# Optimization experiments

Measured on AMD Instinct MI355X. Metric: run time of the kernel, lower is better.

The kernel has to match this reference:

```python
import jax, jax.numpy as jnp
import numpy as np

N_NODES = 100000
N_EDGES = 200000
N_FEAT = 300
HIDDEN = 300
NUM_GRAPHS = 2048
NUM_BOND_TYPE = 6
NUM_BOND_DIR = 3


def setup_inputs() -> dict:
    key = jax.random.key(0)
    ks = jax.random.split(key, 12)
    x = jax.random.normal(ks[0], (N_NODES, N_FEAT), dtype=jnp.float32)
    edge_index = jax.random.randint(ks[1], (2, N_EDGES), 0, N_NODES, dtype=jnp.int64)
    edge_attr = jax.random.randint(ks[2], (N_EDGES, 2), 0, NUM_BOND_DIR, dtype=jnp.int64)
    batch = jnp.sort(jax.random.randint(ks[3], (N_NODES,), 0, NUM_GRAPHS, dtype=jnp.int64))
    s = 1.0 / np.sqrt(N_FEAT)
    emb1 = jax.random.normal(ks[4], (NUM_BOND_TYPE, N_FEAT), dtype=jnp.float32) * s
    emb2 = jax.random.normal(ks[5], (NUM_BOND_DIR, N_FEAT), dtype=jnp.float32) * s
    W1 = jax.random.normal(ks[6], (N_FEAT, 2 * N_FEAT), dtype=jnp.float32) * s
    b1 = jnp.zeros((2 * N_FEAT,), dtype=jnp.float32)
    W2 = jax.random.normal(ks[7], (2 * N_FEAT, HIDDEN), dtype=jnp.float32) * (1.0 / np.sqrt(2 * N_FEAT))
    b2 = jnp.zeros((HIDDEN,), dtype=jnp.float32)
    Wfc = jax.random.normal(ks[8], (HIDDEN, HIDDEN), dtype=jnp.float32) * (1.0 / np.sqrt(HIDDEN))
    bfc = jnp.zeros((HIDDEN,), dtype=jnp.float32)
    return {"x": x, "edge_index": edge_index, "edge_attr": edge_attr, "batch": batch,
            "emb1": emb1, "emb2": emb2, "W1": W1, "b1": b1, "W2": W2, "b2": b2,
            "Wfc": Wfc, "bfc": bfc}


def reference(x, edge_index, edge_attr, batch, emb1, emb2, W1, b1, W2, b2, Wfc, bfc):
    n = x.shape[0]
    # add_self_loops(fill_value=0): append N self edges with zero edge_attr
    loop = jnp.arange(n, dtype=edge_index.dtype)
    src = jnp.concatenate([edge_index[0], loop])  # [E+N]
    dst = jnp.concatenate([edge_index[1], loop])
    ea = jnp.concatenate([edge_attr, jnp.zeros((n, 2), dtype=edge_attr.dtype)], axis=0)
    # edge embeddings (shared by both conv layers)
    edge_emb = emb1[ea[:, 0]] + emb2[ea[:, 1]]  # [E+N, F]

    def mlp(h):
        return jax.nn.relu(h @ W1 + b1) @ W2 + b2

    def gin(h):
        # message: x_j + edge_emb, scatter-add at target nodes, then shared MLP
        msg = h[src] + edge_emb
        aggr = jax.ops.segment_sum(msg, dst, num_segments=n)
        return mlp(aggr)

    h = jax.nn.relu(gin(x))
    h = jax.nn.relu(gin(h))
    # global_add_pool over graphs in batch
    g = jax.ops.segment_sum(h, batch, num_segments=NUM_GRAPHS)  # [G, H]
    return g @ Wfc + bfc
```

## Files before the change

### kernel.cpp

```cpp
#include <hip/hip_runtime.h>
#include <hip/hip_bf16.h>

#define NFEAT 300
#define KP 320
#define NGRAPH 2048
#define N1P 640
#define N2P 384
#define NTD 18
#define SCAN_B 2048

typedef __bf16 bf16x8 __attribute__((ext_vector_type(8)));
typedef float  f32x4  __attribute__((ext_vector_type(4)));
typedef unsigned short u16x8 __attribute__((ext_vector_type(8)));

__device__ __forceinline__ unsigned short f2b(float v) {
    union { float f; unsigned u; } x; x.f = v;
    unsigned r = x.u + 0x7fff + ((x.u >> 16) & 1);
    return (unsigned short)(r >> 16);
}
__device__ __forceinline__ float b2f(unsigned short u) {
    union { unsigned u; float f; } x; x.u = ((unsigned)u) << 16;
    return x.f;
}

#define GLD_LDS16(g, l)                                                        \
    __builtin_amdgcn_global_load_lds(                                          \
        (const __attribute__((address_space(1))) void*)(g),                    \
        (__attribute__((address_space(3))) void*)(l), 16, 0, 0)

__global__ __launch_bounds__(256) void k_embc(
    const float* __restrict__ emb1, const float* __restrict__ emb2,
    float* __restrict__ embc)
{
    int t = blockIdx.x * blockDim.x + threadIdx.x;
    if (t >= NTD * KP) return;
    int td = t / KP, c = t % KP;
    int t1 = td / 3, d = td % 3;
    embc[t] = (c < NFEAT) ? emb1[t1 * NFEAT + c] + emb2[d * NFEAT + c] : 0.f;
}

__global__ __launch_bounds__(256) void k_cvtX(
    const float* __restrict__ x, unsigned short* __restrict__ xb, int n, int Mpad)
{
    int idx = blockIdx.x * blockDim.x + threadIdx.x;
    if (idx >= Mpad * (KP / 8)) return;
    int row = idx / (KP / 8), c0 = (idx % (KP / 8)) * 8;
    unsigned short o[8];
#pragma unroll
    for (int j = 0; j < 8; ++j) {
        int col = c0 + j;
        float v = (row < n && col < NFEAT) ? x[(size_t)row * NFEAT + col] : 0.f;
        o[j] = f2b(v);
    }
    *(uint4*)&xb[(size_t)row * KP + c0] = *(uint4*)o;
}

__global__ __launch_bounds__(256) void k_zero(int* __restrict__ p, int n)
{
    int i = blockIdx.x * blockDim.x + threadIdx.x;
    if (i < n) p[i] = 0;
}

__global__ __launch_bounds__(256) void k_deg(
    const int* __restrict__ ei, int* __restrict__ deg, int E)
{
    int e = blockIdx.x * blockDim.x + threadIdx.x;
    if (e >= E) return;
    atomicAdd(&deg[ei[E + e]], 1);
}

__global__ __launch_bounds__(256) void k_scan1(
    const int* __restrict__ deg, int* __restrict__ offsets,
    int* __restrict__ bsum, int n)
{
    __shared__ int sh[256];
    int tid = threadIdx.x;
    int base = blockIdx.x * SCAN_B + tid * 8;
    int v[8], run = 0;
#pragma unroll
    for (int j = 0; j < 8; ++j) {
        int i = base + j;
        v[j] = (i < n) ? deg[i] : 0;
        run += v[j];
        v[j] = run;
    }
    sh[tid] = run;
    __syncthreads();
    for (int off = 1; off < 256; off <<= 1) {
        int t = (tid >= off) ? sh[tid - off] : 0;
        __syncthreads();
        sh[tid] += t;
        __syncthreads();
    }
    int excl = sh[tid] - run;
#pragma unroll
    for (int j = 0; j < 8; ++j) {
        int i = base + j;
        if (i < n) offsets[i + 1] = excl + v[j];
    }
    if (tid == 0) bsum[blockIdx.x] = sh[255];
}

__global__ void k_scan2(int* __restrict__ bsum, int nb, int* __restrict__ offsets)
{
    if (threadIdx.x == 0 && blockIdx.x == 0) {
        int run = 0;
        for (int b = 0; b < nb; ++b) { int t = bsum[b]; bsum[b] = run; run += t; }
        offsets[0] = 0;
    }
}

__global__ __launch_bounds__(256) void k_scan3(
    const int* __restrict__ deg, int* __restrict__ offsets,
    const int* __restrict__ bsum, int* __restrict__ cursor, int n)
{
    int i = blockIdx.x * blockDim.x + threadIdx.x;
    if (i >= n) return;
    int fin = offsets[i + 1] + bsum[i / SCAN_B];
    offsets[i + 1] = fin;
    cursor[i] = fin - deg[i];
}

__global__ __launch_bounds__(256) void k_fill(
    const int* __restrict__ ei, const int* __restrict__ ea,
    int* __restrict__ cursor, int* __restrict__ edgerec, int E)
{
    int e = blockIdx.x * blockDim.x + threadIdx.x;
    if (e >= E) return;
    int dst = ei[E + e];
    int pos = atomicAdd(&cursor[dst], 1);
    int src = ei[e];
    int td  = ea[2 * e] * 3 + ea[2 * e + 1];
    edgerec[pos] = src | (td << 20);
}

__global__ __launch_bounds__(256) void k_aggr(
    const unsigned short* __restrict__ h,
    const int* __restrict__ offsets, const int* __restrict__ edgerec,
    const float* __restrict__ embc,
    unsigned short* __restrict__ Ab, int n, int Mpad)
{
    int idx = blockIdx.x * blockDim.x + threadIdx.x;
    if (idx >= Mpad * (KP / 8)) return;
    int v = idx / (KP / 8), c0 = (idx % (KP / 8)) * 8;
    unsigned short* outp = &Ab[(size_t)v * KP + c0];
    if (v >= n) {
        *(uint4*)outp = make_uint4(0, 0, 0, 0);
        return;
    }
    float acc[8];
    u16x8 hv = *(const u16x8*)&h[(size_t)v * KP + c0];
    const float* e0 = embc + c0;
#pragma unroll
    for (int j = 0; j < 8; ++j) acc[j] = b2f(hv[j]) + e0[j];

    int beg = offsets[v], end = offsets[v + 1];
    for (int e = beg; e < end; ++e) {
        int rec = edgerec[e];
        int src = rec & 0xFFFFF;
        int td  = rec >> 20;
        u16x8 hs = *(const u16x8*)&h[(size_t)src * KP + c0];
        const float* ee = embc + td * KP + c0;
#pragma unroll
        for (int j = 0; j < 8; ++j) acc[j] += b2f(hs[j]) + ee[j];
    }
    unsigned short o[8];
#pragma unroll
    for (int j = 0; j < 8; ++j) o[j] = f2b(acc[j]);
    *(uint4*)outp = *(uint4*)o;
}

__global__ __launch_bounds__(256) void k_cvtW(
    const float* __restrict__ W, unsigned short* __restrict__ Wt,
    int rows, int cols, int Kpad, int Npad)
{
    int t = blockIdx.x * blockDim.x + threadIdx.x;
    if (t >= Npad * Kpad) return;
    int nn = t / Kpad, k = t % Kpad;
    float v = (k < rows && nn < cols) ? W[(size_t)k * cols + nn] : 0.f;
    Wt[t] = f2b(v);
}

__global__ __launch_bounds__(256) void k_gemm(
    const unsigned short* __restrict__ Ag, const unsigned short* __restrict__ Bg,
    const float* __restrict__ bias, int bias_n,
    unsigned short* __restrict__ C, int ldc, int store_cols,
    int K, int npass, int MT)
{
    __shared__ unsigned short smem[8192];

    int tid  = threadIdx.x;
    int lane = tid & 63, wave = tid >> 6;

    int l    = blockIdx.x;
    int xcd  = l & 7;
    int j    = l >> 3;
    int ncol = j % npass;
    int panel= (j / npass) * 8 + xcd;
    if (panel >= MT) return;
    int m0 = panel * 128;

    int wm = (wave >> 1) * 64, wn = (wave & 1) * 64;
    int fr = lane & 15, fq = lane >> 4;
    int colq = lane & 15, rq = (lane >> 4) * 4;

    const unsigned short* Abase = Ag + (size_t)m0 * K;
    const unsigned short* Bbase = Bg + (size_t)ncol * 128 * K;

    int c0 = tid, c1 = 256 + tid;
    size_t aoff0 = (size_t)(c0 >> 2) * K + 8 * ((c0 & 3) ^ ((c0 >> 3) & 3));
    size_t aoff1 = (size_t)(c1 >> 2) * K + 8 * ((c1 & 3) ^ ((c1 >> 3) & 3));

    int fswz = 8 * (fq ^ ((fr >> 1) & 3));

    f32x4 acc[4][4];
#pragma unroll
    for (int i = 0; i < 4; ++i)
#pragma unroll
        for (int jj = 0; jj < 4; ++jj)
            acc[i][jj] = (f32x4){0.f, 0.f, 0.f, 0.f};

    for (int k0 = 0; k0 < K; k0 += 32) {
        GLD_LDS16(Abase + aoff0 + k0, &smem[c0 * 8]);
        GLD_LDS16(Abase + aoff1 + k0, &smem[c1 * 8]);
        GLD_LDS16(Bbase + aoff0 + k0, &smem[4096 + c0 * 8]);
        GLD_LDS16(Bbase + aoff1 + k0, &smem[4096 + c1 * 8]);
        __syncthreads();

        bf16x8 af[4], bfv[4];
#pragma unroll
        for (int i = 0; i < 4; ++i) {
            af[i]  = *(const bf16x8*)&smem[(wm + i * 16 + fr) * 32 + fswz];
            bfv[i] = *(const bf16x8*)&smem[4096 + (wn + i * 16 + fr) * 32 + fswz];
        }
#pragma unroll
        for (int i = 0; i < 4; ++i)
#pragma unroll
            for (int jj = 0; jj < 4; ++jj)
                acc[i][jj] = __builtin_amdgcn_mfma_f32_16x16x32_bf16(
                    af[i], bfv[jj], acc[i][jj], 0, 0, 0);
        __syncthreads();
    }

#pragma unroll
    for (int ch = 0; ch < 2; ++ch) {
        if ((wn >> 6) == ch) {
#pragma unroll
            for (int jj = 0; jj < 4; ++jj) {
                int lc  = jj * 16 + colq;
                int col = ncol * 128 + wn + jj * 16 + colq;
                float bv = (col < bias_n) ? bias[col] : 0.f;
#pragma unroll
                for (int i = 0; i < 4; ++i) {
                    int rbase = wm + i * 16 + rq;
#pragma unroll
                    for (int r = 0; r < 4; ++r) {
                        float v = fmaxf(acc[i][jj][r] + bv, 0.f);
                        smem[(rbase + r) * 64 + lc] = f2b(v);
                    }
                }
            }
        }
        __syncthreads();
        int cbase = ncol * 128 + ch * 64;
        if (cbase < store_cols) {
#pragma unroll
            for (int i = 0; i < 4; ++i) {
                int idx = i * 256 + tid;
                int row = idx >> 3, c8 = idx & 7;
                *(uint4*)&C[(size_t)(m0 + row) * ldc + cbase + c8 * 8] =
                    *(uint4*)&smem[row * 64 + c8 * 8];
            }
        }
        __syncthreads();
    }
}

__global__ __launch_bounds__(256) void k_pool(
    const unsigned short* __restrict__ H, const int* __restrict__ batch,
    float* __restrict__ g, int n)
{
    int gid = blockIdx.x;
    int lo = 0, hi = n;
    while (lo < hi) { int mid = (lo + hi) >> 1; if (batch[mid] < gid) lo = mid + 1; else hi = mid; }
    int start = lo;
    hi = n;
    while (lo < hi) { int mid = (lo + hi) >> 1; if (batch[mid] < gid + 1) lo = mid + 1; else hi = mid; }
    int end = lo;

    for (int f = threadIdx.x; f < NFEAT; f += blockDim.x) {
        float acc = 0.f;
        for (int v = start; v < end; ++v) acc += b2f(H[(size_t)v * KP + f]);
        g[(size_t)gid * NFEAT + f] = acc;
    }
}

__global__ __launch_bounds__(256) void k_final(
    const float* __restrict__ g, const float* __restrict__ Wfc,
    const float* __restrict__ bfc, float* __restrict__ out)
{
    int idx = blockIdx.x * blockDim.x + threadIdx.x;
    if (idx >= NGRAPH * NFEAT) return;
    int r = idx / NFEAT, c = idx % NFEAT;
    float acc = bfc[c];
    for (int k = 0; k < NFEAT; ++k)
        acc = fmaf(g[(size_t)r * NFEAT + k], Wfc[(size_t)k * NFEAT + c], acc);
    out[idx] = acc;
}

extern "C" void kernel_launch(void* const* d_in, const int* in_sizes, int n_in,
                              void* d_out, int out_size, void* d_ws, size_t ws_size,
                              hipStream_t stream)
{
    const float* x    = (const float*)d_in[0];
    const int*   ei   = (const int*)  d_in[1];
    const int*   ea   = (const int*)  d_in[2];
    const int*   batch= (const int*)  d_in[3];
    const float* emb1 = (const float*)d_in[4];
    const float* emb2 = (const float*)d_in[5];
    const float* W1   = (const float*)d_in[6];
    const float* b1   = (const float*)d_in[7];
    const float* W2   = (const float*)d_in[8];
    const float* b2   = (const float*)d_in[9];
    const float* Wfc  = (const float*)d_in[10];
    const float* bfc  = (const float*)d_in[11];
    float* out = (float*)d_out;

    int n = in_sizes[0] / NFEAT;
    int E = in_sizes[1] / 2;
    int MT   = (n + 127) / 128;
    int Mpad = MT * 128;
    int MT8  = ((MT + 7) / 8) * 8;

    char* p = (char*)d_ws;
    auto take = [&](size_t bytes) { char* r = p; p += (bytes + 255) & ~(size_t)255; return r; };
    unsigned short* T    = (unsigned short*)take((size_t)Mpad * N1P * 2);
    unsigned short* xb   = T;
    unsigned short* Ab   = (unsigned short*)take((size_t)Mpad * KP * 2);
    unsigned short* Hb   = (unsigned short*)take((size_t)Mpad * KP * 2);
    unsigned short* Wt1  = (unsigned short*)take((size_t)N1P * KP * 2);
    unsigned short* Wt2  = (unsigned short*)take((size_t)N2P * N1P * 2);
    float*          embc = (float*)take((size_t)NTD * KP * 4);
    float*          g    = (float*)take((size_t)NGRAPH * NFEAT * 4);
    int*            deg  = (int*)take((size_t)n * 4);
    int*            offs = (int*)take((size_t)(n + 1) * 4);
    int*            curs = (int*)take((size_t)n * 4);
    int*            erec = (int*)take((size_t)E * 4);
    int*            bsum = (int*)take(256 * 4);

    dim3 blk(256);
    int chunkThreads = Mpad * (KP / 8);
    int chunkBlocks  = (chunkThreads + 255) / 256;
    int nb = (n + SCAN_B - 1) / SCAN_B;

    k_cvtW<<<(N1P * KP + 255) / 256, blk, 0, stream>>>(W1, Wt1, NFEAT, 600, KP, N1P);
    k_cvtW<<<(N2P * N1P + 255) / 256, blk, 0, stream>>>(W2, Wt2, 600, NFEAT, N1P, N2P);
    k_embc<<<(NTD * KP + 255) / 256, blk, 0, stream>>>(emb1, emb2, embc);
    k_cvtX<<<chunkBlocks, blk, 0, stream>>>(x, xb, n, Mpad);

    k_zero <<<(n + 255) / 256, blk, 0, stream>>>(deg, n);
    k_deg  <<<(E + 255) / 256, blk, 0, stream>>>(ei, deg, E);
    k_scan1<<<nb, blk, 0, stream>>>(deg, offs, bsum, n);
    k_scan2<<<1, 64, 0, stream>>>(bsum, nb, offs);
    k_scan3<<<(n + 255) / 256, blk, 0, stream>>>(deg, offs, bsum, curs, n);
    k_fill <<<(E + 255) / 256, blk, 0, stream>>>(ei, ea, curs, erec, E);

    k_aggr<<<chunkBlocks, blk, 0, stream>>>(xb, offs, erec, embc, Ab, n, Mpad);
    k_gemm<<<MT8 * (N1P / 128), blk, 0, stream>>>(Ab, Wt1, b1, 600, T, N1P, N1P, KP, N1P / 128, MT);
    k_gemm<<<MT8 * (N2P / 128), blk, 0, stream>>>(T, Wt2, b2, NFEAT, Hb, KP, KP, N1P, N2P / 128, MT);

    k_aggr<<<chunkBlocks, blk, 0, stream>>>(Hb, offs, erec, embc, Ab, n, Mpad);
    k_gemm<<<MT8 * (N1P / 128), blk, 0, stream>>>(Ab, Wt1, b1, 600, T, N1P, N1P, KP, N1P / 128, MT);
    k_gemm<<<MT8 * (N2P / 128), blk, 0, stream>>>(T, Wt2, b2, NFEAT, Hb, KP, KP, N1P, N2P / 128, MT);

    k_pool <<<NGRAPH, blk, 0, stream>>>(Hb, batch, g, n);
    k_final<<<(NGRAPH * NFEAT + 255) / 256, blk, 0, stream>>>(g, Wfc, bfc, out);
}
```

Baseline: 750.3 us.

## Fuse input conversion into first aggregation, double-buffer GEMM LDS, vectorize pooling

Drops the separate fp32-to-bf16 conversion pass over x. The first aggregation now gathers fp32 rows of x directly and writes bf16 results. The GEMM k-loop double-buffers its LDS tiles, so the next tile's global-to-LDS loads are issued while the current tile's MFMAs run; this doubles shared memory per block. Pooling now uses 64-thread blocks with 8-wide bf16 vector loads per thread instead of strided scalar loads. The first aggregation also reads twice the bytes per gathered row.

```diff
diff --git a/kernel.cpp b/kernel.cpp
--- a/kernel.cpp
+++ b/kernel.cpp
@@ -39,22 +39,6 @@
     embc[t] = (c < NFEAT) ? emb1[t1 * NFEAT + c] + emb2[d * NFEAT + c] : 0.f;
 }
 
-__global__ __launch_bounds__(256) void k_cvtX(
-    const float* __restrict__ x, unsigned short* __restrict__ xb, int n, int Mpad)
-{
-    int idx = blockIdx.x * blockDim.x + threadIdx.x;
-    if (idx >= Mpad * (KP / 8)) return;
-    int row = idx / (KP / 8), c0 = (idx % (KP / 8)) * 8;
-    unsigned short o[8];
-#pragma unroll
-    for (int j = 0; j < 8; ++j) {
-        int col = c0 + j;
-        float v = (row < n && col < NFEAT) ? x[(size_t)row * NFEAT + col] : 0.f;
-        o[j] = f2b(v);
-    }
-    *(uint4*)&xb[(size_t)row * KP + c0] = *(uint4*)o;
-}
-
 __global__ __launch_bounds__(256) void k_zero(int* __restrict__ p, int n)
 {
     int i = blockIdx.x * blockDim.x + threadIdx.x;
@@ -134,7 +118,7 @@
     edgerec[pos] = src | (td << 20);
 }
 
-__global__ __launch_bounds__(256) void k_aggr(
+__global__ __launch_bounds__(256) void k_aggr_b16(
     const unsigned short* __restrict__ h,
     const int* __restrict__ offsets, const int* __restrict__ edgerec,
     const float* __restrict__ embc,
@@ -170,6 +154,64 @@
     *(uint4*)outp = *(uint4*)o;
 }
 
+__global__ __launch_bounds__(256) void k_aggr_f32(
+    const float* __restrict__ x,
+    const int* __restrict__ offsets, const int* __restrict__ edgerec,
+    const float* __restrict__ embc,
+    unsigned short* __restrict__ Ab, int n, int Mpad)
+{
+    int idx = blockIdx.x * blockDim.x + threadIdx.x;
+    if (idx >= Mpad * (KP / 8)) return;
+    int v = idx / (KP / 8), c0 = (idx % (KP / 8)) * 8;
+    unsigned short* outp = &Ab[(size_t)v * KP + c0];
+    if (v >= n || c0 >= 304) {
+        if (v < Mpad) *(uint4*)outp = make_uint4(0, 0, 0, 0);
+        return;
+    }
+    bool full = (c0 + 8 <= NFEAT);
+
+    float acc[8];
+    {
+        const float* row = x + (size_t)v * NFEAT + c0;
+        if (full) {
+            float4 a = *(const float4*)row, b = *(const float4*)(row + 4);
+            acc[0] = a.x; acc[1] = a.y; acc[2] = a.z; acc[3] = a.w;
+            acc[4] = b.x; acc[5] = b.y; acc[6] = b.z; acc[7] = b.w;
+        } else {
+#pragma unroll
+            for (int j = 0; j < 8; ++j)
+                acc[j] = (c0 + j < NFEAT) ? row[j] : 0.f;
+        }
+        const float* e0 = embc + c0;
+#pragma unroll
+        for (int j = 0; j < 8; ++j) acc[j] += e0[j];
+    }
+
+    int beg = offsets[v], end = offsets[v + 1];
+    for (int e = beg; e < end; ++e) {
+        int rec = edgerec[e];
+        int src = rec & 0xFFFFF;
+        int td  = rec >> 20;
+        const float* row = x + (size_t)src * NFEAT + c0;
+        const float* ee  = embc + td * KP + c0;
+        if (full) {
+            float4 a = *(const float4*)row, b = *(const float4*)(row + 4);
+            acc[0] += a.x + ee[0]; acc[1] += a.y + ee[1];
+            acc[2] += a.z + ee[2]; acc[3] += a.w + ee[3];
+            acc[4] += b.x + ee[4]; acc[5] += b.y + ee[5];
+            acc[6] += b.z + ee[6]; acc[7] += b.w + ee[7];
+        } else {
+#pragma unroll
+            for (int j = 0; j < 8; ++j)
+                acc[j] += ((c0 + j < NFEAT) ? row[j] : 0.f) + ee[j];
+        }
+    }
+    unsigned short o[8];
+#pragma unroll
+    for (int j = 0; j < 8; ++j) o[j] = f2b(acc[j]);
+    *(uint4*)outp = *(uint4*)o;
+}
+
 __global__ __launch_bounds__(256) void k_cvtW(
     const float* __restrict__ W, unsigned short* __restrict__ Wt,
     int rows, int cols, int Kpad, int Npad)
@@ -187,7 +229,7 @@
     unsigned short* __restrict__ C, int ldc, int store_cols,
     int K, int npass, int MT)
 {
-    __shared__ unsigned short smem[8192];
+    __shared__ unsigned short smem[16384];
 
     int tid  = threadIdx.x;
     int lane = tid & 63, wave = tid >> 6;
@@ -220,25 +262,37 @@
         for (int jj = 0; jj < 4; ++jj)
             acc[i][jj] = (f32x4){0.f, 0.f, 0.f, 0.f};
 
-    for (int k0 = 0; k0 < K; k0 += 32) {
-        GLD_LDS16(Abase + aoff0 + k0, &smem[c0 * 8]);
-        GLD_LDS16(Abase + aoff1 + k0, &smem[c1 * 8]);
-        GLD_LDS16(Bbase + aoff0 + k0, &smem[4096 + c0 * 8]);
-        GLD_LDS16(Bbase + aoff1 + k0, &smem[4096 + c1 * 8]);
-        __syncthreads();
+    int niter = K >> 5;
+
+    GLD_LDS16(Abase + aoff0, &smem[c0 * 8]);
+    GLD_LDS16(Abase + aoff1, &smem[c1 * 8]);
+    GLD_LDS16(Bbase + aoff0, &smem[4096 + c0 * 8]);
+    GLD_LDS16(Bbase + aoff1, &smem[4096 + c1 * 8]);
+    __syncthreads();
+
+    for (int i = 0; i < niter; ++i) {
+        int cur = (i & 1) << 13;
+        int nxt = 8192 - cur;
+        if (i + 1 < niter) {
+            int k0 = (i + 1) * 32;
+            GLD_LDS16(Abase + aoff0 + k0, &smem[nxt + c0 * 8]);
+            GLD_LDS16(Abase + aoff1 + k0, &smem[nxt + c1 * 8]);
+            GLD_LDS16(Bbase + aoff0 + k0, &smem[nxt + 4096 + c0 * 8]);
+            GLD_LDS16(Bbase + aoff1 + k0, &smem[nxt + 4096 + c1 * 8]);
+        }
 
         bf16x8 af[4], bfv[4];
 #pragma unroll
-        for (int i = 0; i < 4; ++i) {
-            af[i]  = *(const bf16x8*)&smem[(wm + i * 16 + fr) * 32 + fswz];
-            bfv[i] = *(const bf16x8*)&smem[4096 + (wn + i * 16 + fr) * 32 + fswz];
-        }
-#pragma unroll
-        for (int i = 0; i < 4; ++i)
+        for (int i2 = 0; i2 < 4; ++i2) {
+            af[i2]  = *(const bf16x8*)&smem[cur + (wm + i2 * 16 + fr) * 32 + fswz];
+            bfv[i2] = *(const bf16x8*)&smem[cur + 4096 + (wn + i2 * 16 + fr) * 32 + fswz];
+        }
+#pragma unroll
+        for (int i2 = 0; i2 < 4; ++i2)
 #pragma unroll
             for (int jj = 0; jj < 4; ++jj)
-                acc[i][jj] = __builtin_amdgcn_mfma_f32_16x16x32_bf16(
-                    af[i], bfv[jj], acc[i][jj], 0, 0, 0);
+                acc[i2][jj] = __builtin_amdgcn_mfma_f32_16x16x32_bf16(
+                    af[i2], bfv[jj], acc[i2][jj], 0, 0, 0);
         __syncthreads();
     }
 
@@ -276,7 +330,7 @@
     }
 }
 
-__global__ __launch_bounds__(256) void k_pool(
+__global__ __launch_bounds__(64) void k_pool(
     const unsigned short* __restrict__ H, const int* __restrict__ batch,
     float* __restrict__ g, int n)
 {
@@ -288,11 +342,20 @@
     while (lo < hi) { int mid = (lo + hi) >> 1; if (batch[mid] < gid + 1) lo = mid + 1; else hi = mid; }
     int end = lo;
 
-    for (int f = threadIdx.x; f < NFEAT; f += blockDim.x) {
-        float acc = 0.f;
-        for (int v = start; v < end; ++v) acc += b2f(H[(size_t)v * KP + f]);
-        g[(size_t)gid * NFEAT + f] = acc;
-    }
+    int ch = threadIdx.x;
+    if (ch >= KP / 8) return;
+    int c0 = ch * 8;
+    float acc[8];
+#pragma unroll
+    for (int j = 0; j < 8; ++j) acc[j] = 0.f;
+    for (int v = start; v < end; ++v) {
+        u16x8 hv = *(const u16x8*)&H[(size_t)v * KP + c0];
+#pragma unroll
+        for (int j = 0; j < 8; ++j) acc[j] += b2f(hv[j]);
+    }
+#pragma unroll
+    for (int j = 0; j < 8; ++j)
+        if (c0 + j < NFEAT) g[(size_t)gid * NFEAT + c0 + j] = acc[j];
 }
 
 __global__ __launch_bounds__(256) void k_final(
@@ -335,7 +398,6 @@
     char* p = (char*)d_ws;
     auto take = [&](size_t bytes) { char* r = p; p += (bytes + 255) & ~(size_t)255; return r; };
     unsigned short* T    = (unsigned short*)take((size_t)Mpad * N1P * 2);
-    unsigned short* xb   = T;
     unsigned short* Ab   = (unsigned short*)take((size_t)Mpad * KP * 2);
     unsigned short* Hb   = (unsigned short*)take((size_t)Mpad * KP * 2);
     unsigned short* Wt1  = (unsigned short*)take((size_t)N1P * KP * 2);
@@ -356,7 +418,6 @@
     k_cvtW<<<(N1P * KP + 255) / 256, blk, 0, stream>>>(W1, Wt1, NFEAT, 600, KP, N1P);
     k_cvtW<<<(N2P * N1P + 255) / 256, blk, 0, stream>>>(W2, Wt2, 600, NFEAT, N1P, N2P);
     k_embc<<<(NTD * KP + 255) / 256, blk, 0, stream>>>(emb1, emb2, embc);
-    k_cvtX<<<chunkBlocks, blk, 0, stream>>>(x, xb, n, Mpad);
 
     k_zero <<<(n + 255) / 256, blk, 0, stream>>>(deg, n);
     k_deg  <<<(E + 255) / 256, blk, 0, stream>>>(ei, deg, E);
@@ -365,14 +426,14 @@
     k_scan3<<<(n + 255) / 256, blk, 0, stream>>>(deg, offs, bsum, curs, n);
     k_fill <<<(E + 255) / 256, blk, 0, stream>>>(ei, ea, curs, erec, E);
 
-    k_aggr<<<chunkBlocks, blk, 0, stream>>>(xb, offs, erec, embc, Ab, n, Mpad);
+    k_aggr_f32<<<chunkBlocks, blk, 0, stream>>>(x, offs, erec, embc, Ab, n, Mpad);
     k_gemm<<<MT8 * (N1P / 128), blk, 0, stream>>>(Ab, Wt1, b1, 600, T, N1P, N1P, KP, N1P / 128, MT);
     k_gemm<<<MT8 * (N2P / 128), blk, 0, stream>>>(T, Wt2, b2, NFEAT, Hb, KP, KP, N1P, N2P / 128, MT);
 
-    k_aggr<<<chunkBlocks, blk, 0, stream>>>(Hb, offs, erec, embc, Ab, n, Mpad);
+    k_aggr_b16<<<chunkBlocks, blk, 0, stream>>>(Hb, offs, erec, embc, Ab, n, Mpad);
     k_gemm<<<MT8 * (N1P / 128), blk, 0, stream>>>(Ab, Wt1, b1, 600, T, N1P, N1P, KP, N1P / 128, MT);
     k_gemm<<<MT8 * (N2P / 128), blk, 0, stream>>>(T, Wt2, b2, NFEAT, Hb, KP, KP, N1P, N2P / 128, MT);
 
-    k_pool <<<NGRAPH, blk, 0, stream>>>(Hb, batch, g, n);
+    k_pool <<<NGRAPH, 64, 0, stream>>>(Hb, batch, g, n);
     k_final<<<(NGRAPH * NFEAT + 255) / 256, blk, 0, stream>>>(g, Wfc, bfc, out);
 }
```

New measurement: 750.5 us. About the same (+0.0%).
